# Performance work log

Measured on AMD Instinct MI355X. Metric: run time of the kernel, lower is better.

The kernel has to match this reference:

```python
import jax, jax.numpy as jnp
import numpy as np

N_HEAD = 16
SPARSE_TOPK = 64
NEG_INF = float('-inf')


def setup_inputs() -> dict:
    key = jax.random.key(0)
    ks = jax.random.split(key, 12)
    B, T, C = 4, 1024, 1024
    s = 0.02
    q = jax.random.normal(ks[0], (B, T, C), jnp.float32)
    kv = jax.random.normal(ks[1], (B, T, C), jnp.float32)  # forward asserts k == v
    tgt_mask = jnp.tril(jnp.ones((T, T), jnp.bool_)).reshape(1, 1, T, T)
    inp = {'q': q, 'k': kv, 'v': kv, 'tgt_mask': tgt_mask}
    for i, n in enumerate(['Wq', 'Wk', 'Wv', 'Wo']):
        inp[n] = jax.random.normal(ks[2 + i], (C, C), jnp.float32) * s
    for i, n in enumerate(['bq', 'bk', 'bv', 'bo']):
        inp[n] = jax.random.normal(ks[6 + i], (C,), jnp.float32) * s
    return inp


def reference(q, k, v, tgt_mask, Wq, Wk, Wv, Wo, bq, bk, bv, bo):
    B, T, C = q.shape
    H = N_HEAD
    hd = C // H
    scale = 1.0 / np.sqrt(hd).astype(np.float32)
    # QKV projections -> [B, H, T, hd]
    qh = (q @ Wq + bq).reshape(B, T, H, hd).transpose(0, 2, 1, 3)
    kh = (k @ Wk + bk).reshape(B, T, H, hd).transpose(0, 2, 1, 3)
    vh = (v @ Wv + bv).reshape(B, T, H, hd).transpose(0, 2, 1, 3)
    # full attention scores [B, H, T, T]
    att = jnp.einsum('bhtd,bhsd->bhts', qh, kh) * scale
    # causal mask: masked_fill where tgt_mask == 0
    att = jnp.where(tgt_mask[:, :, :T, :T], att, NEG_INF)
    # top-k sparse pruning: keep entries >= k-th largest per row (ties kept)
    top, _ = jax.lax.top_k(att, SPARSE_TOPK)
    vk = top[..., -1:]  # [B, H, T, 1]
    att = jnp.where(att < vk, NEG_INF, att)
    att = jax.nn.softmax(att, axis=-1)
    # dropout is identity in eval (p=0.0)
    y = jnp.einsum('bhts,bhsd->bhtd', att, vh)
    y = y.transpose(0, 2, 1, 3).reshape(B, T, C)
    return y @ Wo + bo
```

## Files before the change

kernel.cpp:

```cpp
#include <hip/hip_runtime.h>
#include <hip/hip_bf16.h>
#include <math.h>

typedef __attribute__((ext_vector_type(8))) short short8;
typedef __attribute__((ext_vector_type(4))) float f32x4;
typedef __attribute__((ext_vector_type(4))) int int4v;

#define SCL 0.1803368801111204f

static __device__ __forceinline__ unsigned short f2bf(float f) {
  unsigned u = __float_as_uint(f);
  u = u + 0x7FFFu + ((u >> 16) & 1u);
  return (unsigned short)(u >> 16);
}
static __device__ __forceinline__ unsigned pack2(float lo, float hi) {
  const unsigned ul = __float_as_uint(lo) + 0x8000u;
  const unsigned uh = __float_as_uint(hi) + 0x8000u;
  return (uh & 0xFFFF0000u) | (ul >> 16);
}

static __device__ __forceinline__ unsigned keyof(float x) {
  unsigned u = __float_as_uint(x);
  return (u & 0x80000000u) ? ~u : (u | 0x80000000u);
}
static __device__ __forceinline__ float keyinv(unsigned k) {
  unsigned u = (k & 0x80000000u) ? (k & 0x7FFFFFFFu) : ~k;
  return __uint_as_float(u);
}

static __device__ __forceinline__ int saddr(int r, int cc) {
  return (((r << 9) + cc) << 2) ^ ((r & 7) << 4);
}
static __device__ __forceinline__ int paddr(int r, int c) {
  return ((r << 11) + (c << 1)) ^ ((r & 7) << 4);
}

static __device__ __forceinline__ void gld_lds16(const unsigned short* g, unsigned short* l) {
  __builtin_amdgcn_global_load_lds(
      (const __attribute__((address_space(1))) void*)g,
      (__attribute__((address_space(3))) void*)l, 16, 0, 0);
}

__global__ __launch_bounds__(256) void wtrans4_k(const float* __restrict__ Wq,
                                                 const float* __restrict__ Wk,
                                                 const float* __restrict__ Wv,
                                                 const float* __restrict__ Wo,
                                                 unsigned short* __restrict__ Wqt,
                                                 unsigned short* __restrict__ Wkt,
                                                 unsigned short* __restrict__ Wvt,
                                                 unsigned short* __restrict__ Wot) {
  const int z = blockIdx.z;
  const float* W = (z == 0) ? Wq : (z == 1) ? Wk : (z == 2) ? Wv : Wo;
  unsigned short* Wt = (z == 0) ? Wqt : (z == 1) ? Wkt : (z == 2) ? Wvt : Wot;
  __shared__ float tile[32][33];
  const int tx = threadIdx.x, ty = threadIdx.y;
  const int x0 = blockIdx.x * 32, y0 = blockIdx.y * 32;
#pragma unroll
  for (int j = 0; j < 4; ++j)
    tile[ty + j * 8][tx] = W[(y0 + ty + j * 8) * 1024 + x0 + tx];
  __syncthreads();
#pragma unroll
  for (int j = 0; j < 4; ++j)
    Wt[(x0 + ty + j * 8) * 1024 + (y0 + tx)] = f2bf(tile[tx][ty + j * 8]);
}

template <int MODE>
static __device__ __forceinline__ void gemm_bodyF(unsigned short* As0, unsigned short* Bs0,
                                                  unsigned short* As1, unsigned short* Bs1,
                                                  const float* __restrict__ A,
                                                  const unsigned short* __restrict__ Bt,
                                                  const float* __restrict__ bias,
                                                  void* __restrict__ out) {
  const int tid = threadIdx.x;
  const int lane = tid & 63, w = tid >> 6;
  const int wr = w >> 1, wc = w & 1;
  const int m0 = blockIdx.y * 128, n0 = blockIdx.x * 128;
  const int l15 = lane & 15, l4 = lane >> 4;
  f32x4 acc[4][4] = {};
  const int r0 = tid >> 2, s0 = (tid & 3) * 8;
  const int r1 = r0 + 64;
  const float* gA0 = A + (m0 + r0) * 1024 + s0;
  const float* gA1 = A + (m0 + r1) * 1024 + s0;
  const unsigned short* gB0 = Bt + (n0 + r0) * 1024 + s0;
  const unsigned short* gB1 = Bt + (n0 + r1) * 1024 + s0;
  const int oA0 = r0 * 32 + s0, oA1 = r1 * 32 + s0;

  {
    const f32x4 a0 = *(const f32x4*)(gA0);
    const f32x4 a1 = *(const f32x4*)(gA0 + 4);
    const f32x4 c0 = *(const f32x4*)(gA1);
    const f32x4 c1 = *(const f32x4*)(gA1 + 4);
    gld_lds16(gB0, Bs0 + oA0);
    gld_lds16(gB1, Bs0 + oA1);
    int4v pa, pb;
    pa[0] = (int)pack2(a0[0], a0[1]); pa[1] = (int)pack2(a0[2], a0[3]);
    pa[2] = (int)pack2(a1[0], a1[1]); pa[3] = (int)pack2(a1[2], a1[3]);
    pb[0] = (int)pack2(c0[0], c0[1]); pb[1] = (int)pack2(c0[2], c0[3]);
    pb[2] = (int)pack2(c1[0], c1[1]); pb[3] = (int)pack2(c1[2], c1[3]);
    *(int4v*)(As0 + oA0) = pa;
    *(int4v*)(As0 + oA1) = pb;
  }
  __syncthreads();

  for (int kt = 0; kt < 32; ++kt) {
    f32x4 a0, a1, c0, c1;
    if (kt < 31) {
      const int k0n = (kt + 1) * 32;
      a0 = *(const f32x4*)(gA0 + k0n);
      a1 = *(const f32x4*)(gA0 + k0n + 4);
      c0 = *(const f32x4*)(gA1 + k0n);
      c1 = *(const f32x4*)(gA1 + k0n + 4);
      unsigned short* Bsn = (kt & 1) ? Bs0 : Bs1;
      gld_lds16(gB0 + k0n, Bsn + oA0);
      gld_lds16(gB1 + k0n, Bsn + oA1);
    }
    const unsigned short* Asc = (kt & 1) ? As1 : As0;
    const unsigned short* Bsc = (kt & 1) ? Bs1 : Bs0;
    short8 af[4], bfr[4];
#pragma unroll
    for (int i = 0; i < 4; ++i) {
      af[i]  = *(const short8*)(Asc + (wr * 64 + i * 16 + l15) * 32 + l4 * 8);
      bfr[i] = *(const short8*)(Bsc + (wc * 64 + i * 16 + l15) * 32 + l4 * 8);
    }
#pragma unroll
    for (int i = 0; i < 4; ++i)
#pragma unroll
      for (int j = 0; j < 4; ++j)
        acc[i][j] = __builtin_amdgcn_mfma_f32_16x16x32_bf16(af[i], bfr[j], acc[i][j], 0, 0, 0);
    if (kt < 31) {
      unsigned short* Asn = (kt & 1) ? As0 : As1;
      int4v pa, pb;
      pa[0] = (int)pack2(a0[0], a0[1]); pa[1] = (int)pack2(a0[2], a0[3]);
      pa[2] = (int)pack2(a1[0], a1[1]); pa[3] = (int)pack2(a1[2], a1[3]);
      pb[0] = (int)pack2(c0[0], c0[1]); pb[1] = (int)pack2(c0[2], c0[3]);
      pb[2] = (int)pack2(c1[0], c1[1]); pb[3] = (int)pack2(c1[2], c1[3]);
      *(int4v*)(Asn + oA0) = pa;
      *(int4v*)(Asn + oA1) = pb;
    }
    __syncthreads();
  }
#pragma unroll
  for (int i = 0; i < 4; ++i) {
#pragma unroll
    for (int j = 0; j < 4; ++j) {
      const int n = n0 + wc * 64 + j * 16 + l15;
      const float bv = bias[n];
#pragma unroll
      for (int r = 0; r < 4; ++r) {
        const int m = m0 + wr * 64 + i * 16 + l4 * 4 + r;
        const float v = acc[i][j][r] + bv;
        const int bb = m >> 10, t = m & 1023, hh = n >> 6, dd = n & 63;
        const unsigned short bfv = f2bf(v);
        if (MODE == 0)
          ((unsigned short*)out)[(((bb << 4) + hh) * 1024 + t) * 64 + dd] = bfv;
        else
          ((unsigned short*)out)[(((bb << 4) + hh) * 64 + dd) * 1024 + t] = bfv;
      }
    }
  }
}

__global__ __launch_bounds__(256) void gemm_qkv_k(
    const float* q, const float* k, const float* v,
    const unsigned short* Wqt, const unsigned short* Wkt, const unsigned short* Wvt,
    const float* bq, const float* bk, const float* bv,
    unsigned short* Qh, unsigned short* Kh, unsigned short* Vth) {
  __shared__ unsigned short As0[128 * 32], Bs0[128 * 32], As1[128 * 32], Bs1[128 * 32];
  const int z = blockIdx.z;
  const float* A           = (z == 0) ? q   : ((z == 1) ? k   : v);
  const unsigned short* Bt = (z == 0) ? Wqt : ((z == 1) ? Wkt : Wvt);
  const float* bias        = (z == 0) ? bq  : ((z == 1) ? bk  : bv);
  if (z == 2) gemm_bodyF<1>(As0, Bs0, As1, Bs1, A, Bt, bias, Vth);
  else        gemm_bodyF<0>(As0, Bs0, As1, Bs1, A, Bt, bias, z ? Kh : Qh);
}

__global__ __launch_bounds__(256) void gemm_out_k(const unsigned short* __restrict__ Y,
                                                  const unsigned short* __restrict__ Wot,
                                                  const float* __restrict__ bo,
                                                  float* __restrict__ out) {
  __shared__ unsigned short As0[128 * 32], Bs0[128 * 32], As1[128 * 32], Bs1[128 * 32];
  const int tid = threadIdx.x;
  const int lane = tid & 63, w = tid >> 6;
  const int wr = w >> 1, wc = w & 1;
  const int m0 = blockIdx.y * 128, n0 = blockIdx.x * 128;
  const int l15 = lane & 15, l4 = lane >> 4;
  f32x4 acc[4][4] = {};
  const int r0 = tid >> 2, s0 = (tid & 3) * 8;
  const int r1 = r0 + 64;
  const unsigned short* gA0 = Y + (m0 + r0) * 1024 + s0;
  const unsigned short* gA1 = Y + (m0 + r1) * 1024 + s0;
  const unsigned short* gB0 = Wot + (n0 + r0) * 1024 + s0;
  const unsigned short* gB1 = Wot + (n0 + r1) * 1024 + s0;
  const int oA0 = r0 * 32 + s0, oA1 = r1 * 32 + s0;

  gld_lds16(gA0, As0 + oA0);
  gld_lds16(gA1, As0 + oA1);
  gld_lds16(gB0, Bs0 + oA0);
  gld_lds16(gB1, Bs0 + oA1);
  __syncthreads();

  for (int kt = 0; kt < 32; ++kt) {
    if (kt < 31) {
      const int k0n = (kt + 1) * 32;
      unsigned short* Asn = (kt & 1) ? As0 : As1;
      unsigned short* Bsn = (kt & 1) ? Bs0 : Bs1;
      gld_lds16(gA0 + k0n, Asn + oA0);
      gld_lds16(gA1 + k0n, Asn + oA1);
      gld_lds16(gB0 + k0n, Bsn + oA0);
      gld_lds16(gB1 + k0n, Bsn + oA1);
    }
    const unsigned short* Asc = (kt & 1) ? As1 : As0;
    const unsigned short* Bsc = (kt & 1) ? Bs1 : Bs0;
    short8 af[4], bfr[4];
#pragma unroll
    for (int i = 0; i < 4; ++i) {
      af[i]  = *(const short8*)(Asc + (wr * 64 + i * 16 + l15) * 32 + l4 * 8);
      bfr[i] = *(const short8*)(Bsc + (wc * 64 + i * 16 + l15) * 32 + l4 * 8);
    }
#pragma unroll
    for (int i = 0; i < 4; ++i)
#pragma unroll
      for (int j = 0; j < 4; ++j)
        acc[i][j] = __builtin_amdgcn_mfma_f32_16x16x32_bf16(af[i], bfr[j], acc[i][j], 0, 0, 0);
    __syncthreads();
  }
#pragma unroll
  for (int i = 0; i < 4; ++i) {
#pragma unroll
    for (int j = 0; j < 4; ++j) {
      const int n = n0 + wc * 64 + j * 16 + l15;
      const float bv = bo[n];
#pragma unroll
      for (int r = 0; r < 4; ++r) {
        const int m = m0 + wr * 64 + i * 16 + l4 * 4 + r;
        out[m * 1024 + n] = acc[i][j][r] + bv;
      }
    }
  }
}

template <int NVAL, bool FORCE>
static __device__ __forceinline__ void process_row(char* __restrict__ smem, float (&v)[NVAL],
                                                   const int r, const int Lr, const int Lpad,
                                                   const int lane, float* __restrict__ RED2) {
  float lm = v[0];
#pragma unroll
  for (int i = 1; i < NVAL; ++i) lm = fmaxf(lm, v[i]);
  float mx = lm;
#pragma unroll
  for (int o = 32; o; o >>= 1) mx = fmaxf(mx, __shfl_xor(mx, o));

  float thr = -INFINITY;
  if (FORCE || Lr > 64) {
    float mn = lm;
#pragma unroll
    for (int o = 32; o; o >>= 1) mn = fminf(mn, __shfl_xor(mn, o));
    unsigned lo = (unsigned)__builtin_amdgcn_readfirstlane((int)keyof(mn));
    unsigned hi = (unsigned)__builtin_amdgcn_readfirstlane((int)keyof(mx)) + 1u;
    int cl = Lr, ch = 0, alt = 0;
    while (hi - lo > 1u) {
      const unsigned span = hi - lo;
      unsigned off;
      if (alt) off = span >> 1;
      else {
        const float fr = (float)(cl - 64) / (float)(cl - ch);
        off = (unsigned)(fr * (float)span);
        if (off < 1u) off = 1u;
        if (off > span - 1u) off = span - 1u;
      }
      alt ^= 1;
      const unsigned mid = lo + off;
      const float tm = keyinv(mid);
      int cnt = 0;
#pragma unroll
      for (int i = 0; i < NVAL; ++i) cnt += (int)__popcll(__ballot(v[i] >= tm));
      if (cnt >= 64) { lo = mid; cl = cnt; if (cnt == 64) break; }
      else { hi = mid; ch = cnt; }
    }
    thr = keyinv(lo);
  }

  float s = 0.f;
  unsigned pk[NVAL / 2];
#pragma unroll
  for (int p = 0; p < NVAL / 2; ++p) {
    const float p0 = (v[2 * p]     >= thr) ? exp2f(v[2 * p]     - mx) : 0.f;
    const float p1 = (v[2 * p + 1] >= thr) ? exp2f(v[2 * p + 1] - mx) : 0.f;
    s += p0 + p1;
    pk[p] = (unsigned)f2bf(p0) | ((unsigned)f2bf(p1) << 16);
  }
#pragma unroll
  for (int o = 32; o; o >>= 1) s += __shfl_xor(s, o);
  if (lane == 0) RED2[r] = 1.f / s;
#pragma unroll
  for (int p = 0; p < NVAL / 2; ++p) {
    const int c = ((p & 3) << 7) + (lane << 1) + ((p >= 4) ? 512 : 0);
    if (c < Lpad) *(unsigned*)(smem + paddr(r, c)) = pk[p];
  }
}

static __device__ __forceinline__ void pv_phase16(char* __restrict__ smem,
                                                  const unsigned short* __restrict__ Vh,
                                                  unsigned short* __restrict__ Y,
                                                  const int t0, const int h, const int b,
                                                  const int lane, const int w, const int Lpad) {
  const int l15 = lane & 15, l4 = lane >> 4;
  float* RED3 = (float*)(smem + 32768);
  float* RED2 = (float*)(smem + 32768 + 13056);
  const int nST = Lpad >> 5;
  const int q = (nST + 3) >> 2;
  const int kseg = w >> 2;
  const int d0 = (w & 3) * 16;
  int lo = kseg * q, hi = lo + q;
  if (lo > nST) lo = nST;
  if (hi > nST) hi = nST;
  f32x4 acc = {0.f, 0.f, 0.f, 0.f};
  for (int st = lo; st < hi; ++st) {
    const int sb = st * 32 + l4 * 8;
    const short8 paf = *(const short8*)(smem + paddr(l15, sb));
    const short8 vb = *(const short8*)(Vh + (d0 + l15) * 1024 + sb);
    acc = __builtin_amdgcn_mfma_f32_16x16x32_bf16(paf, vb, acc, 0, 0, 0);
  }
  if (kseg > 0) {
#pragma unroll
    for (int r = 0; r < 4; ++r)
      RED3[((kseg - 1) * 16 + l4 * 4 + r) * 68 + d0 + l15] = acc[r];
  }
  __syncthreads();
  if (kseg == 0) {
    const int d = (h << 6) + d0 + l15;
#pragma unroll
    for (int r = 0; r < 4; ++r) {
      const int row = l4 * 4 + r;
      const int col = d0 + l15;
      float s = acc[r] + RED3[(row) * 68 + col] + RED3[(16 + row) * 68 + col] +
                RED3[(32 + row) * 68 + col];
      Y[((b << 10) + t0 + row) * 1024 + d] = f2bf(s * RED2[row]);
    }
  }
}

__global__ __launch_bounds__(1024, 8) void attn_hv_k(const unsigned short* __restrict__ Q,
                                                     const unsigned short* __restrict__ K,
                                                     const unsigned short* __restrict__ Vt,
                                                     unsigned short* __restrict__ Y) {
  extern __shared__ __align__(16) char smem[];
  const int tid = threadIdx.x, lane = tid & 63, w = tid >> 6;
  const int t0 = 1008 - 16 * (int)blockIdx.x;
  const int h = blockIdx.y, b = blockIdx.z;
  const unsigned short* Qp = Q + (((b * 16 + h) * 1024) + t0) * 64;
  const unsigned short* Kh = K + (b * 16 + h) * 65536;
  const unsigned short* Vh = Vt + (b * 16 + h) * 65536;
  const int L = t0 + 16;
  const int Lpad = (L + 31) & ~31;
  const int nCT = L >> 4;
  const int l15 = lane & 15, l4 = lane >> 4;
  float* RED2 = (float*)(smem + 32768 + 13056);

  const short8 aq0 = *(const short8*)(Qp + l15 * 64 + l4 * 8);
  const short8 aq1 = *(const short8*)(Qp + l15 * 64 + 32 + l4 * 8);

  auto qk_chunk = [&](int tlo, int thi) {
    for (int ct = tlo + w; ct < thi; ct += 16) {
      const int c0 = ct * 16;
      const short8 kb0 = *(const short8*)(Kh + (c0 + l15) * 64 + l4 * 8);
      const short8 kb1 = *(const short8*)(Kh + (c0 + l15) * 64 + 32 + l4 * 8);
      f32x4 acc = {0.f, 0.f, 0.f, 0.f};
      acc = __builtin_amdgcn_mfma_f32_16x16x32_bf16(aq0, kb0, acc, 0, 0, 0);
      acc = __builtin_amdgcn_mfma_f32_16x16x32_bf16(aq1, kb1, acc, 0, 0, 0);
      const int c = c0 + l15, cc = c & 511;
      if (ct == nCT - 1) {
#pragma unroll
        for (int r = 0; r < 4; ++r) {
          const int row = l4 * 4 + r;
          *(float*)(smem + saddr(row, cc)) = (c <= t0 + row) ? acc[r] * SCL : -INFINITY;
        }
      } else {
#pragma unroll
        for (int r = 0; r < 4; ++r)
          *(float*)(smem + saddr(l4 * 4 + r, cc)) = acc[r] * SCL;
      }
    }
  };

  qk_chunk(0, 32);
  __syncthreads();
  const int Lr = t0 + w + 1;
  float v[16];
#pragma unroll
  for (int p = 0; p < 4; ++p) {
    const int c = (p << 7) + (lane << 1);
    const float2 t = *(const float2*)(smem + saddr(w, c));
    v[2 * p] = t.x; v[2 * p + 1] = t.y;
  }
  __syncthreads();
  qk_chunk(32, nCT);
  __syncthreads();
#pragma unroll
  for (int p = 0; p < 4; ++p) {
    const int cc = (p << 7) + (lane << 1);
    const float2 t = *(const float2*)(smem + saddr(w, cc));
    const bool vld = (cc + 512) < L;
    v[8 + 2 * p] = vld ? t.x : -INFINITY;
    v[9 + 2 * p] = vld ? t.y : -INFINITY;
  }
  process_row<16, true>(smem, v, w, Lr, Lpad, lane, RED2);
  __syncthreads();
  pv_phase16(smem, Vh, Y, t0, h, b, lane, w, Lpad);
}

__global__ __launch_bounds__(1024, 8) void attn_lt_k(const unsigned short* __restrict__ Q,
                                                     const unsigned short* __restrict__ K,
                                                     const unsigned short* __restrict__ Vt,
                                                     unsigned short* __restrict__ Y) {
  extern __shared__ __align__(16) char smem[];
  const int tid = threadIdx.x, lane = tid & 63, w = tid >> 6;
  const int t0 = 496 - 16 * (int)blockIdx.x;
  const int h = blockIdx.y, b = blockIdx.z;
  const unsigned short* Qp = Q + (((b * 16 + h) * 1024) + t0) * 64;
  const unsigned short* Kh = K + (b * 16 + h) * 65536;
  const unsigned short* Vh = Vt + (b * 16 + h) * 65536;
  const int L = t0 + 16;
  const int Lpad = (L + 31) & ~31;
  const int nCT = L >> 4;
  const int l15 = lane & 15, l4 = lane >> 4;
  float* RED2 = (float*)(smem + 32768 + 13056);

  const short8 aq0 = *(const short8*)(Qp + l15 * 64 + l4 * 8);
  const short8 aq1 = *(const short8*)(Qp + l15 * 64 + 32 + l4 * 8);

  for (int ct = w; ct < nCT; ct += 16) {
    const int c0 = ct * 16;
    const short8 kb0 = *(const short8*)(Kh + (c0 + l15) * 64 + l4 * 8);
    const short8 kb1 = *(const short8*)(Kh + (c0 + l15) * 64 + 32 + l4 * 8);
    f32x4 acc = {0.f, 0.f, 0.f, 0.f};
    acc = __builtin_amdgcn_mfma_f32_16x16x32_bf16(aq0, kb0, acc, 0, 0, 0);
    acc = __builtin_amdgcn_mfma_f32_16x16x32_bf16(aq1, kb1, acc, 0, 0, 0);
    const int c = c0 + l15, cc = c & 511;
    if (ct == nCT - 1) {
#pragma unroll
      for (int r = 0; r < 4; ++r) {
        const int row = l4 * 4 + r;
        *(float*)(smem + saddr(row, cc)) = (c <= t0 + row) ? acc[r] * SCL : -INFINITY;
      }
    } else {
#pragma unroll
      for (int r = 0; r < 4; ++r)
        *(float*)(smem + saddr(l4 * 4 + r, cc)) = acc[r] * SCL;
    }
  }
  __syncthreads();

  const int Lr = t0 + w + 1;
  float v[8];
#pragma unroll
  for (int p = 0; p < 4; ++p) {
    const int c = (p << 7) + (lane << 1);
    const float2 t = *(const float2*)(smem + saddr(w, c));
    const bool vld = c < L;
    v[2 * p]     = vld ? t.x : -INFINITY;
    v[2 * p + 1] = vld ? t.y : -INFINITY;
  }
  process_row<8, false>(smem, v, w, Lr, Lpad, lane, RED2);
  __syncthreads();
  pv_phase16(smem, Vh, Y, t0, h, b, lane, w, Lpad);
}

extern "C" void kernel_launch(void* const* d_in, const int* in_sizes, int n_in,
                              void* d_out, int out_size, void* d_ws, size_t ws_size,
                              hipStream_t stream) {
  const float* q  = (const float*)d_in[0];
  const float* k  = (const float*)d_in[1];
  const float* v  = (const float*)d_in[2];
  const float* Wq = (const float*)d_in[4];
  const float* Wk = (const float*)d_in[5];
  const float* Wv = (const float*)d_in[6];
  const float* Wo = (const float*)d_in[7];
  const float* bq = (const float*)d_in[8];
  const float* bk = (const float*)d_in[9];
  const float* bv = (const float*)d_in[10];
  const float* bo = (const float*)d_in[11];

  char* ws = (char*)d_ws;
  const size_t MB = 1u << 20;
  unsigned short* Y   = (unsigned short*)(ws + 0 * MB);
  unsigned short* Wqt = (unsigned short*)(ws + 24 * MB);
  unsigned short* Wkt = (unsigned short*)(ws + 26 * MB);
  unsigned short* Wvt = (unsigned short*)(ws + 28 * MB);
  unsigned short* Wot = (unsigned short*)(ws + 30 * MB);
  unsigned short* Qh  = (unsigned short*)(ws + 32 * MB);
  unsigned short* Kh  = (unsigned short*)(ws + 40 * MB);
  unsigned short* Vth = (unsigned short*)(ws + 48 * MB);

  wtrans4_k<<<dim3(32, 32, 4), dim3(32, 8), 0, stream>>>(Wq, Wk, Wv, Wo, Wqt, Wkt, Wvt, Wot);
  gemm_qkv_k<<<dim3(8, 32, 3), 256, 0, stream>>>(q, k, v, Wqt, Wkt, Wvt,
                                                 bq, bk, bv, Qh, Kh, Vth);
  attn_hv_k<<<dim3(32, 16, 4), 1024, 45888, stream>>>(Qh, Kh, Vth, Y);
  attn_lt_k<<<dim3(32, 16, 4), 1024, 45888, stream>>>(Qh, Kh, Vth, Y);
  gemm_out_k<<<dim3(8, 32), 256, 0, stream>>>(Y, Wot, bo, (float*)d_out);
}
```

Baseline: 231.9 us.

## Merge attention kernels and seed top-k threshold search with Gaussian quantile guess

```diff
diff --git a/kernel.cpp b/kernel.cpp
--- a/kernel.cpp
+++ b/kernel.cpp
@@ -239,26 +239,136 @@
   }
 }
 
-template <int NVAL, bool FORCE>
-static __device__ __forceinline__ void process_row(char* __restrict__ smem, float (&v)[NVAL],
-                                                   const int r, const int Lr, const int Lpad,
-                                                   const int lane, float* __restrict__ RED2) {
+__global__ __launch_bounds__(1024, 8) void attn_k(const unsigned short* __restrict__ Q,
+                                                  const unsigned short* __restrict__ K,
+                                                  const unsigned short* __restrict__ Vt,
+                                                  unsigned short* __restrict__ Y) {
+  extern __shared__ __align__(16) char smem[];
+  const int tid = threadIdx.x, lane = tid & 63, w = tid >> 6;
+  const int t0 = 1008 - 16 * (int)blockIdx.x;
+  const int h = blockIdx.y, b = blockIdx.z;
+  const unsigned short* Qp = Q + (((b * 16 + h) * 1024) + t0) * 64;
+  const unsigned short* Kh = K + (b * 16 + h) * 65536;
+  const unsigned short* Vh = Vt + (b * 16 + h) * 65536;
+  const int L = t0 + 16;
+  const int Lpad = (L + 31) & ~31;
+  const int nCT = L >> 4;
+  const bool full = (L > 512);
+  const int l15 = lane & 15, l4 = lane >> 4;
+  float* RED3 = (float*)(smem + 32768);
+  float* RED2 = (float*)(smem + 32768 + 13056);
+
+  const short8 aq0 = *(const short8*)(Qp + l15 * 64 + l4 * 8);
+  const short8 aq1 = *(const short8*)(Qp + l15 * 64 + 32 + l4 * 8);
+
+  auto qk_tiles = [&](int tlo, int thi) {
+    for (int ct = tlo + w; ct < thi; ct += 16) {
+      const int c0 = ct * 16;
+      const short8 kb0 = *(const short8*)(Kh + (c0 + l15) * 64 + l4 * 8);
+      const short8 kb1 = *(const short8*)(Kh + (c0 + l15) * 64 + 32 + l4 * 8);
+      f32x4 acc = {0.f, 0.f, 0.f, 0.f};
+      acc = __builtin_amdgcn_mfma_f32_16x16x32_bf16(aq0, kb0, acc, 0, 0, 0);
+      acc = __builtin_amdgcn_mfma_f32_16x16x32_bf16(aq1, kb1, acc, 0, 0, 0);
+      const int c = c0 + l15, cc = c & 511;
+      if (ct == nCT - 1) {
+#pragma unroll
+        for (int r = 0; r < 4; ++r) {
+          const int row = l4 * 4 + r;
+          *(float*)(smem + saddr(row, cc)) = (c <= t0 + row) ? acc[r] * SCL : -INFINITY;
+        }
+      } else {
+#pragma unroll
+        for (int r = 0; r < 4; ++r)
+          *(float*)(smem + saddr(l4 * 4 + r, cc)) = acc[r] * SCL;
+      }
+    }
+  };
+
+  qk_tiles(0, full ? 32 : nCT);
+  __syncthreads();
+
+  const int Lr = t0 + w + 1;
+  float v[16];
+#pragma unroll
+  for (int p = 0; p < 4; ++p) {
+    const int c = (p << 7) + (lane << 1);
+    const float2 t = *(const float2*)(smem + saddr(w, c));
+    const bool vld = full || (c < L);
+    v[2 * p]     = vld ? t.x : -INFINITY;
+    v[2 * p + 1] = vld ? t.y : -INFINITY;
+  }
+  if (full) {
+    __syncthreads();
+    qk_tiles(32, nCT);
+    __syncthreads();
+#pragma unroll
+    for (int p = 0; p < 4; ++p) {
+      const int cc = (p << 7) + (lane << 1);
+      const float2 t = *(const float2*)(smem + saddr(w, cc));
+      const bool vld = (cc + 512) < L;
+      v[8 + 2 * p] = vld ? t.x : -INFINITY;
+      v[9 + 2 * p] = vld ? t.y : -INFINITY;
+    }
+  } else {
+#pragma unroll
+    for (int i = 8; i < 16; ++i) v[i] = -INFINITY;
+  }
+
   float lm = v[0];
-#pragma unroll
-  for (int i = 1; i < NVAL; ++i) lm = fmaxf(lm, v[i]);
-  float mx = lm;
-#pragma unroll
-  for (int o = 32; o; o >>= 1) mx = fmaxf(mx, __shfl_xor(mx, o));
+  float s1 = 0.f, s2 = 0.f;
+#pragma unroll
+  for (int i = 0; i < 16; ++i) {
+    if (i) lm = fmaxf(lm, v[i]);
+    const bool good = v[i] != -INFINITY;
+    const float x = good ? v[i] : 0.f;
+    s1 += x;
+    s2 += x * x;
+  }
+  float mx = lm, mn = lm;
+#pragma unroll
+  for (int o = 32; o; o >>= 1) {
+    mx = fmaxf(mx, __shfl_xor(mx, o));
+    mn = fminf(mn, __shfl_xor(mn, o));
+    s1 += __shfl_xor(s1, o);
+    s2 += __shfl_xor(s2, o);
+  }
+
+  auto countge = [&](float tm) {
+    int cnt = 0;
+#pragma unroll
+    for (int i = 0; i < 8; ++i) cnt += (int)__popcll(__ballot(v[i] >= tm));
+    if (full) {
+#pragma unroll
+      for (int i = 8; i < 16; ++i) cnt += (int)__popcll(__ballot(v[i] >= tm));
+    }
+    return cnt;
+  };
 
   float thr = -INFINITY;
-  if (FORCE || Lr > 64) {
-    float mn = lm;
-#pragma unroll
-    for (int o = 32; o; o >>= 1) mn = fminf(mn, __shfl_xor(mn, o));
+  if (Lr > 64) {
     unsigned lo = (unsigned)__builtin_amdgcn_readfirstlane((int)keyof(mn));
     unsigned hi = (unsigned)__builtin_amdgcn_readfirstlane((int)keyof(mx)) + 1u;
-    int cl = Lr, ch = 0, alt = 0;
-    while (hi - lo > 1u) {
+    int cl = Lr, ch = 0;
+    {
+      const float fl = (float)Lr;
+      const float mu = s1 / fl;
+      const float var = fmaxf(s2 / fl - mu * mu, 1e-12f);
+      const float sd = sqrtf(var);
+      const float qq = 64.f / fl;
+      const float pp = fminf(qq, 1.f - qq);
+      const float ttv = sqrtf(-2.f * logf(fmaxf(pp, 1e-6f)));
+      float zz = ttv - (2.30753f + 0.27061f * ttv) /
+                           (1.f + 0.99229f * ttv + 0.04481f * ttv * ttv);
+      if (qq > 0.5f) zz = -zz;
+      unsigned k0 = (unsigned)__builtin_amdgcn_readfirstlane((int)keyof(mu + sd * zz));
+      if (k0 <= lo) k0 = lo + 1u;
+      if (k0 >= hi) k0 = hi - 1u;
+      const int cnt = countge(keyinv(k0));
+      if (cnt >= 64) { lo = k0; cl = cnt; if (cnt == 64) hi = k0 + 1u; }
+      else { hi = k0; ch = cnt; }
+    }
+    int alt = 0;
+    for (int it = 0; it < 64 && (hi - lo) > 1u; ++it) {
       const unsigned span = hi - lo;
       unsigned off;
       if (alt) off = span >> 1;
@@ -270,52 +380,57 @@
       }
       alt ^= 1;
       const unsigned mid = lo + off;
-      const float tm = keyinv(mid);
-      int cnt = 0;
-#pragma unroll
-      for (int i = 0; i < NVAL; ++i) cnt += (int)__popcll(__ballot(v[i] >= tm));
-      if (cnt >= 64) { lo = mid; cl = cnt; if (cnt == 64) break; }
+      const int cnt = countge(keyinv(mid));
+      if (cnt >= 64) { lo = mid; cl = cnt; if (cnt == 64) hi = mid + 1u; }
       else { hi = mid; ch = cnt; }
     }
     thr = keyinv(lo);
   }
 
   float s = 0.f;
-  unsigned pk[NVAL / 2];
-#pragma unroll
-  for (int p = 0; p < NVAL / 2; ++p) {
+  unsigned pk[8];
+#pragma unroll
+  for (int p = 0; p < 4; ++p) {
     const float p0 = (v[2 * p]     >= thr) ? exp2f(v[2 * p]     - mx) : 0.f;
     const float p1 = (v[2 * p + 1] >= thr) ? exp2f(v[2 * p + 1] - mx) : 0.f;
     s += p0 + p1;
     pk[p] = (unsigned)f2bf(p0) | ((unsigned)f2bf(p1) << 16);
   }
+  if (full) {
+#pragma unroll
+    for (int p = 4; p < 8; ++p) {
+      const float p0 = (v[2 * p]     >= thr) ? exp2f(v[2 * p]     - mx) : 0.f;
+      const float p1 = (v[2 * p + 1] >= thr) ? exp2f(v[2 * p + 1] - mx) : 0.f;
+      s += p0 + p1;
+      pk[p] = (unsigned)f2bf(p0) | ((unsigned)f2bf(p1) << 16);
+    }
+  }
+#pragma unroll
+  for (int p = 0; p < 4; ++p) {
+    const int c = (p << 7) + (lane << 1);
+    if (c < Lpad) *(unsigned*)(smem + paddr(w, c)) = pk[p];
+  }
+  if (full) {
+#pragma unroll
+    for (int p = 4; p < 8; ++p) {
+      const int c = ((p & 3) << 7) + (lane << 1) + 512;
+      if (c < Lpad) *(unsigned*)(smem + paddr(w, c)) = pk[p];
+    }
+  }
 #pragma unroll
   for (int o = 32; o; o >>= 1) s += __shfl_xor(s, o);
-  if (lane == 0) RED2[r] = 1.f / s;
-#pragma unroll
-  for (int p = 0; p < NVAL / 2; ++p) {
-    const int c = ((p & 3) << 7) + (lane << 1) + ((p >= 4) ? 512 : 0);
-    if (c < Lpad) *(unsigned*)(smem + paddr(r, c)) = pk[p];
-  }
-}
-
-static __device__ __forceinline__ void pv_phase16(char* __restrict__ smem,
-                                                  const unsigned short* __restrict__ Vh,
-                                                  unsigned short* __restrict__ Y,
-                                                  const int t0, const int h, const int b,
-                                                  const int lane, const int w, const int Lpad) {
-  const int l15 = lane & 15, l4 = lane >> 4;
-  float* RED3 = (float*)(smem + 32768);
-  float* RED2 = (float*)(smem + 32768 + 13056);
+  if (lane == 0) RED2[w] = 1.f / s;
+  __syncthreads();
+
   const int nST = Lpad >> 5;
-  const int q = (nST + 3) >> 2;
+  const int qd = (nST + 3) >> 2;
   const int kseg = w >> 2;
   const int d0 = (w & 3) * 16;
-  int lo = kseg * q, hi = lo + q;
-  if (lo > nST) lo = nST;
-  if (hi > nST) hi = nST;
+  int klo = kseg * qd, khi = klo + qd;
+  if (klo > nST) klo = nST;
+  if (khi > nST) khi = nST;
   f32x4 acc = {0.f, 0.f, 0.f, 0.f};
-  for (int st = lo; st < hi; ++st) {
+  for (int st = klo; st < khi; ++st) {
     const int sb = st * 32 + l4 * 8;
     const short8 paf = *(const short8*)(smem + paddr(l15, sb));
     const short8 vb = *(const short8*)(Vh + (d0 + l15) * 1024 + sb);
@@ -333,137 +448,11 @@
     for (int r = 0; r < 4; ++r) {
       const int row = l4 * 4 + r;
       const int col = d0 + l15;
-      float s = acc[r] + RED3[(row) * 68 + col] + RED3[(16 + row) * 68 + col] +
-                RED3[(32 + row) * 68 + col];
-      Y[((b << 10) + t0 + row) * 1024 + d] = f2bf(s * RED2[row]);
-    }
-  }
-}
-
-__global__ __launch_bounds__(1024, 8) void attn_hv_k(const unsigned short* __restrict__ Q,
-                                                     const unsigned short* __restrict__ K,
-                                                     const unsigned short* __restrict__ Vt,
-                                                     unsigned short* __restrict__ Y) {
-  extern __shared__ __align__(16) char smem[];
-  const int tid = threadIdx.x, lane = tid & 63, w = tid >> 6;
-  const int t0 = 1008 - 16 * (int)blockIdx.x;
-  const int h = blockIdx.y, b = blockIdx.z;
-  const unsigned short* Qp = Q + (((b * 16 + h) * 1024) + t0) * 64;
-  const unsigned short* Kh = K + (b * 16 + h) * 65536;
-  const unsigned short* Vh = Vt + (b * 16 + h) * 65536;
-  const int L = t0 + 16;
-  const int Lpad = (L + 31) & ~31;
-  const int nCT = L >> 4;
-  const int l15 = lane & 15, l4 = lane >> 4;
-  float* RED2 = (float*)(smem + 32768 + 13056);
-
-  const short8 aq0 = *(const short8*)(Qp + l15 * 64 + l4 * 8);
-  const short8 aq1 = *(const short8*)(Qp + l15 * 64 + 32 + l4 * 8);
-
-  auto qk_chunk = [&](int tlo, int thi) {
-    for (int ct = tlo + w; ct < thi; ct += 16) {
-      const int c0 = ct * 16;
-      const short8 kb0 = *(const short8*)(Kh + (c0 + l15) * 64 + l4 * 8);
-      const short8 kb1 = *(const short8*)(Kh + (c0 + l15) * 64 + 32 + l4 * 8);
-      f32x4 acc = {0.f, 0.f, 0.f, 0.f};
-      acc = __builtin_amdgcn_mfma_f32_16x16x32_bf16(aq0, kb0, acc, 0, 0, 0);
-      acc = __builtin_amdgcn_mfma_f32_16x16x32_bf16(aq1, kb1, acc, 0, 0, 0);
-      const int c = c0 + l15, cc = c & 511;
-      if (ct == nCT - 1) {
-#pragma unroll
-        for (int r = 0; r < 4; ++r) {
-          const int row = l4 * 4 + r;
-          *(float*)(smem + saddr(row, cc)) = (c <= t0 + row) ? acc[r] * SCL : -INFINITY;
-        }
-      } else {
-#pragma unroll
-        for (int r = 0; r < 4; ++r)
-          *(float*)(smem + saddr(l4 * 4 + r, cc)) = acc[r] * SCL;
-      }
-    }
-  };
-
-  qk_chunk(0, 32);
-  __syncthreads();
-  const int Lr = t0 + w + 1;
-  float v[16];
-#pragma unroll
-  for (int p = 0; p < 4; ++p) {
-    const int c = (p << 7) + (lane << 1);
-    const float2 t = *(const float2*)(smem + saddr(w, c));
-    v[2 * p] = t.x; v[2 * p + 1] = t.y;
-  }
-  __syncthreads();
-  qk_chunk(32, nCT);
-  __syncthreads();
-#pragma unroll
-  for (int p = 0; p < 4; ++p) {
-    const int cc = (p << 7) + (lane << 1);
-    const float2 t = *(const float2*)(smem + saddr(w, cc));
-    const bool vld = (cc + 512) < L;
-    v[8 + 2 * p] = vld ? t.x : -INFINITY;
-    v[9 + 2 * p] = vld ? t.y : -INFINITY;
-  }
-  process_row<16, true>(smem, v, w, Lr, Lpad, lane, RED2);
-  __syncthreads();
-  pv_phase16(smem, Vh, Y, t0, h, b, lane, w, Lpad);
-}
-
-__global__ __launch_bounds__(1024, 8) void attn_lt_k(const unsigned short* __restrict__ Q,
-                                                     const unsigned short* __restrict__ K,
-                                                     const unsigned short* __restrict__ Vt,
-                                                     unsigned short* __restrict__ Y) {
-  extern __shared__ __align__(16) char smem[];
-  const int tid = threadIdx.x, lane = tid & 63, w = tid >> 6;
-  const int t0 = 496 - 16 * (int)blockIdx.x;
-  const int h = blockIdx.y, b = blockIdx.z;
-  const unsigned short* Qp = Q + (((b * 16 + h) * 1024) + t0) * 64;
-  const unsigned short* Kh = K + (b * 16 + h) * 65536;
-  const unsigned short* Vh = Vt + (b * 16 + h) * 65536;
-  const int L = t0 + 16;
-  const int Lpad = (L + 31) & ~31;
-  const int nCT = L >> 4;
-  const int l15 = lane & 15, l4 = lane >> 4;
-  float* RED2 = (float*)(smem + 32768 + 13056);
-
-  const short8 aq0 = *(const short8*)(Qp + l15 * 64 + l4 * 8);
-  const short8 aq1 = *(const short8*)(Qp + l15 * 64 + 32 + l4 * 8);
-
-  for (int ct = w; ct < nCT; ct += 16) {
-    const int c0 = ct * 16;
-    const short8 kb0 = *(const short8*)(Kh + (c0 + l15) * 64 + l4 * 8);
-    const short8 kb1 = *(const short8*)(Kh + (c0 + l15) * 64 + 32 + l4 * 8);
-    f32x4 acc = {0.f, 0.f, 0.f, 0.f};
-    acc = __builtin_amdgcn_mfma_f32_16x16x32_bf16(aq0, kb0, acc, 0, 0, 0);
-    acc = __builtin_amdgcn_mfma_f32_16x16x32_bf16(aq1, kb1, acc, 0, 0, 0);
-    const int c = c0 + l15, cc = c & 511;
-    if (ct == nCT - 1) {
-#pragma unroll
-      for (int r = 0; r < 4; ++r) {
-        const int row = l4 * 4 + r;
-        *(float*)(smem + saddr(row, cc)) = (c <= t0 + row) ? acc[r] * SCL : -INFINITY;
-      }
-    } else {
-#pragma unroll
-      for (int r = 0; r < 4; ++r)
-        *(float*)(smem + saddr(l4 * 4 + r, cc)) = acc[r] * SCL;
-    }
-  }
-  __syncthreads();
-
-  const int Lr = t0 + w + 1;
-  float v[8];
-#pragma unroll
-  for (int p = 0; p < 4; ++p) {
-    const int c = (p << 7) + (lane << 1);
-    const float2 t = *(const float2*)(smem + saddr(w, c));
-    const bool vld = c < L;
-    v[2 * p]     = vld ? t.x : -INFINITY;
-    v[2 * p + 1] = vld ? t.y : -INFINITY;
-  }
-  process_row<8, false>(smem, v, w, Lr, Lpad, lane, RED2);
-  __syncthreads();
-  pv_phase16(smem, Vh, Y, t0, h, b, lane, w, Lpad);
+      float sv = acc[r] + RED3[row * 68 + col] + RED3[(16 + row) * 68 + col] +
+                 RED3[(32 + row) * 68 + col];
+      Y[((b << 10) + t0 + row) * 1024 + d] = f2bf(sv * RED2[row]);
+    }
+  }
 }
 
 extern "C" void kernel_launch(void* const* d_in, const int* in_sizes, int n_in,
@@ -495,7 +484,6 @@
   wtrans4_k<<<dim3(32, 32, 4), dim3(32, 8), 0, stream>>>(Wq, Wk, Wv, Wo, Wqt, Wkt, Wvt, Wot);
   gemm_qkv_k<<<dim3(8, 32, 3), 256, 0, stream>>>(q, k, v, Wqt, Wkt, Wvt,
                                                  bq, bk, bv, Qh, Kh, Vth);
-  attn_hv_k<<<dim3(32, 16, 4), 1024, 45888, stream>>>(Qh, Kh, Vth, Y);
-  attn_lt_k<<<dim3(32, 16, 4), 1024, 45888, stream>>>(Qh, Kh, Vth, Y);
+  attn_k<<<dim3(64, 16, 4), 1024, 45888, stream>>>(Qh, Kh, Vth, Y);
   gemm_out_k<<<dim3(8, 32), 256, 0, stream>>>(Y, Wot, bo, (float*)d_out);
 }
```

After: 234.6 us. Within noise of the previous version (+1.2%).
